# Kernel optimization log

Hardware: AMD Instinct MI355X
Metric: run time of the kernel (lower is better)

Reference implementation:

```python
import jax, jax.numpy as jnp
import numpy as np

B, L, D = 4, 8192, 512


def setup_inputs() -> dict:
    key = jax.random.key(0)
    kx, kwg, kwc = jax.random.split(key, 3)
    x = jax.random.normal(kx, (B, L, D), dtype=jnp.float32)
    # Xavier-uniform init for DxD linears
    bound = float(np.sqrt(6.0 / (D + D)))
    Wg = jax.random.uniform(kwg, (D, D), minval=-bound, maxval=bound, dtype=jnp.float32)
    bg = jnp.ones((D,), dtype=jnp.float32)   # gate bias init to 1.0
    Wc = jax.random.uniform(kwc, (D, D), minval=-bound, maxval=bound, dtype=jnp.float32)
    bc = jnp.zeros((D,), dtype=jnp.float32)
    return {"x": x, "Wg": Wg, "bg": bg, "Wc": Wc, "bc": bc}


def _mingru_scan(gates, cands):
    # h_t = (1 - g_t) * h_{t-1} + g_t * c_t, h_0 = 0
    # linear recurrence h_t = a_t h_{t-1} + b_t with a = 1-g, b = g*c
    a = 1.0 - gates
    b = gates * cands

    def combine(left, right):
        a_l, b_l = left
        a_r, b_r = right
        return a_r * a_l, a_r * b_l + b_r

    _, h = jax.lax.associative_scan(combine, (a, b), axis=1)
    return h


def reference(x, Wg, bg, Wc, bc):
    gates = jax.nn.sigmoid(jnp.einsum('bld,ed->ble', x, Wg) + bg)
    cands = jnp.tanh(jnp.einsum('bld,ed->ble', x, Wc) + bc)
    return _mingru_scan(gates, cands)
```

## Files before the change

kernel.cpp:

```cpp
#include <hip/hip_runtime.h>
#include <stdint.h>
#include <stddef.h>

#define B_ 4
#define L_ 8192
#define D_ 512
#define M_ (B_*L_)
#define K_ 512
#define CHUNK 64
#define NC (L_/CHUNK)

typedef _Float16 f16;
typedef f16 f16x2 __attribute__((ext_vector_type(2)));
typedef f16 f16x4 __attribute__((ext_vector_type(4)));
typedef f16 f16x8 __attribute__((ext_vector_type(8)));
typedef float f32x4 __attribute__((ext_vector_type(4)));

__device__ __forceinline__ void async16(const void* g, void* l) {
  __builtin_amdgcn_global_load_lds(
      (const __attribute__((address_space(1))) uint32_t*)g,
      (__attribute__((address_space(3))) uint32_t*)l,
      16, 0, 0);
}

__global__ __launch_bounds__(256) void prep(const float* __restrict__ x,
                                            const float* __restrict__ Wg,
                                            const float* __restrict__ Wc,
                                            f16* __restrict__ xh,
                                            f16* __restrict__ wp) {
  const int bid = blockIdx.x;
  if (bid < 16384) {
    const int idx = (bid * 256 + threadIdx.x) * 4;
    float4 v = *(const float4*)(x + idx);
    f16x4 o = {(f16)v.x, (f16)v.y, (f16)v.z, (f16)v.w};
    *(f16x4*)(xh + idx) = o;
  } else {
    const int idx = ((bid - 16384) * 256 + threadIdx.x) * 4;
    const float* src = (idx < 262144) ? (Wg + idx) : (Wc + (idx - 262144));
    float4 v = *(const float4*)src;
    f16x4 o = {(f16)v.x, (f16)v.y, (f16)v.z, (f16)v.w};
    *(f16x4*)(wp + idx) = o;
  }
}

__global__ __launch_bounds__(256, 2) void gemm_act(
    const f16* __restrict__ Xh, const f16* __restrict__ Wp,
    const float* __restrict__ bg, const float* __restrict__ bc,
    uint32_t* __restrict__ AC,
    float* __restrict__ cA, float* __restrict__ cB) {
  __shared__ __align__(16) f16 sA[128 * 32];
  __shared__ __align__(16) f16 sBg[128 * 32];
  __shared__ __align__(16) f16 sBc[128 * 32];

  const int tid = threadIdx.x;
  const int id = blockIdx.x;
  const int xcd = id & 7;
  const int slot = id >> 3;
  const int g_ = xcd * 128 + slot;
  const int bm = g_ >> 2;
  const int bn = g_ & 3;

  const int lane = tid & 63;
  const int w = tid >> 6;
  const int wm = w >> 1, wn = w & 1;
  const int l15 = lane & 15, quad = lane >> 4;

  const int srow = tid >> 2;
  const int spc8 = (tid & 3) * 8;
  const f16* gA  = Xh + (size_t)(bm * 128 + srow) * K_ + spc8;
  const f16* gBg = Wp + (size_t)(bn * 128 + srow) * K_ + spc8;
  const f16* gBc = Wp + (size_t)(512 + bn * 128 + srow) * K_ + spc8;
  f16* lA  = sA  + tid * 8;
  f16* lBg = sBg + tid * 8;
  f16* lBc = sBc + tid * 8;

  f32x4 accG[4][4] = {};
  f32x4 accC[4][4] = {};

  for (int k0 = 0; k0 < K_; k0 += 32) {
    async16(gA + k0,  lA);
    async16(gA + (size_t)64 * K_ + k0,  lA  + 64 * 32);
    async16(gBg + k0, lBg);
    async16(gBg + (size_t)64 * K_ + k0, lBg + 64 * 32);
    async16(gBc + k0, lBc);
    async16(gBc + (size_t)64 * K_ + k0, lBc + 64 * 32);
    __syncthreads();

    f16x8 af[4], bgf[4], bcf[4];
#pragma unroll
    for (int i = 0; i < 4; i++)
      af[i]  = *(const f16x8*)(sA  + (wm * 64 + i * 16 + l15) * 32 + quad * 8);
#pragma unroll
    for (int j = 0; j < 4; j++) {
      bgf[j] = *(const f16x8*)(sBg + (wn * 64 + j * 16 + l15) * 32 + quad * 8);
      bcf[j] = *(const f16x8*)(sBc + (wn * 64 + j * 16 + l15) * 32 + quad * 8);
    }
#pragma unroll
    for (int i = 0; i < 4; i++)
#pragma unroll
      for (int j = 0; j < 4; j++) {
        accG[i][j] = __builtin_amdgcn_mfma_f32_16x16x32_f16(af[i], bgf[j], accG[i][j], 0, 0, 0);
        accC[i][j] = __builtin_amdgcn_mfma_f32_16x16x32_f16(af[i], bcf[j], accC[i][j], 0, 0, 0);
      }
    __syncthreads();
  }

  const int c = bm * 2 + wm;
#pragma unroll
  for (int j = 0; j < 4; j++) {
    const int col = bn * 128 + wn * 64 + j * 16 + l15;
    const float bgv = bg[col];
    const float bcv = bc[col];
    float blkP[4], blkQ[4];
#pragma unroll
    for (int i = 0; i < 4; i++) {
      const int mrow = bm * 128 + wm * 64 + i * 16 + quad * 4;
      float P = 1.0f, Q = 0.0f;
#pragma unroll
      for (int r = 0; r < 4; r++) {
        float yg = accG[i][j][r] + bgv;
        float gg = 1.0f / (1.0f + __expf(-yg));
        float yc = accC[i][j][r] + bcv;
        yc = fminf(fmaxf(yc, -15.0f), 15.0f);
        float t = __expf(2.0f * yc);
        float cc = (t - 1.0f) / (t + 1.0f);
        f16x2 p;
        p[0] = (f16)(1.0f - gg);
        p[1] = (f16)(gg * cc);
        *(f16x2*)&AC[(size_t)(mrow + r) * 512 + col] = p;
        const float av = (float)p[0];
        const float bv = (float)p[1];
        Q = fmaf(av, Q, bv);
        P *= av;
      }
      float Pp = __shfl_xor(P, 16);
      float Qp = __shfl_xor(Q, 16);
      float nP = P * Pp;
      float nQ = (quad & 1) ? fmaf(P, Qp, Q) : fmaf(Pp, Q, Qp);
      Pp = __shfl_xor(nP, 32);
      Qp = __shfl_xor(nQ, 32);
      blkP[i] = nP * Pp;
      blkQ[i] = (quad & 2) ? fmaf(nP, Qp, nQ) : fmaf(Pp, nQ, Qp);
    }
    float CP = blkP[0], CQ = blkQ[0];
#pragma unroll
    for (int i = 1; i < 4; i++) {
      CQ = fmaf(blkP[i], CQ, blkQ[i]);
      CP *= blkP[i];
    }
    if (quad == 0) {
      cA[(size_t)c * 512 + col] = CP;
      cB[(size_t)c * 512 + col] = CQ;
    }
  }
}

__global__ __launch_bounds__(256) void scan_apply(
    const uint32_t* __restrict__ AC,
    const float* __restrict__ cA, const float* __restrict__ cB,
    float* __restrict__ out) {
  const int blk = blockIdx.x;
  const int ch = blk & (NC - 1);
  const int bseq = blk >> 7;
  const int d0 = threadIdx.x * 2;

  float h0 = 0.0f, h1 = 0.0f;
  const float* pA = cA + (size_t)(bseq * NC) * 512 + d0;
  const float* pB = cB + (size_t)(bseq * NC) * 512 + d0;
#pragma unroll 4
  for (int cc = 0; cc < ch; cc++) {
    float2 va = *(const float2*)(pA + (size_t)cc * 512);
    float2 vb = *(const float2*)(pB + (size_t)cc * 512);
    h0 = fmaf(va.x, h0, vb.x);
    h1 = fmaf(va.y, h1, vb.y);
  }

  const size_t base = (size_t)blk * CHUNK * 512 + d0;
#pragma unroll 8
  for (int t = 0; t < CHUNK; t++) {
    const size_t i = base + (size_t)t * 512;
    uint2 v = *(const uint2*)&AC[i];
    f16x2 p0 = __builtin_bit_cast(f16x2, v.x);
    f16x2 p1 = __builtin_bit_cast(f16x2, v.y);
    h0 = fmaf((float)p0[0], h0, (float)p0[1]);
    h1 = fmaf((float)p1[0], h1, (float)p1[1]);
    float2 o;
    o.x = h0;
    o.y = h1;
    *(float2*)&out[i] = o;
  }
}

extern "C" void kernel_launch(void* const* d_in, const int* in_sizes, int n_in,
                              void* d_out, int out_size, void* d_ws, size_t ws_size,
                              hipStream_t stream) {
  const float* x  = (const float*)d_in[0];
  const float* Wg = (const float*)d_in[1];
  const float* bg = (const float*)d_in[2];
  const float* Wc = (const float*)d_in[3];
  const float* bc = (const float*)d_in[4];
  float* out = (float*)d_out;

  char* ws = (char*)d_ws;
  f16*      xh = (f16*)(ws);
  f16*      wp = (f16*)(ws + 33554432);
  uint32_t* AC = (uint32_t*)(ws + 34603008);
  float*    cA = (float*)(ws + 101711872);
  float*    cB = (float*)(ws + 102760448);

  prep<<<16896, 256, 0, stream>>>(x, Wg, Wc, xh, wp);
  gemm_act<<<(M_ / 128) * 4, 256, 0, stream>>>(xh, wp, bg, bc, AC, cA, cB);
  scan_apply<<<B_ * NC, 256, 0, stream>>>(AC, cA, cB, out);
}
```

Measured before the change: 208.6 us.

## Fuse x fp32-to-fp16 conversion into GEMM loads and double-buffer LDS tiles

Removes the separate pass that converted x to fp16. The GEMM now loads fp32 x directly into registers, converts it, and writes it to LDS. The K loop is double-buffered: the next tile's loads are issued before the current tile's MFMAs, with manual waitcnt and barriers. This saves a full write and read of the 32MB fp16 x copy, but each GEMM block now reads fp32 x, which is twice the bytes of the fp16 copy, and each tile repeats that read across the 4 column blocks.

```diff
diff --git a/kernel.cpp b/kernel.cpp
--- a/kernel.cpp
+++ b/kernel.cpp
@@ -23,34 +23,24 @@
       16, 0, 0);
 }
 
-__global__ __launch_bounds__(256) void prep(const float* __restrict__ x,
-                                            const float* __restrict__ Wg,
-                                            const float* __restrict__ Wc,
-                                            f16* __restrict__ xh,
-                                            f16* __restrict__ wp) {
-  const int bid = blockIdx.x;
-  if (bid < 16384) {
-    const int idx = (bid * 256 + threadIdx.x) * 4;
-    float4 v = *(const float4*)(x + idx);
-    f16x4 o = {(f16)v.x, (f16)v.y, (f16)v.z, (f16)v.w};
-    *(f16x4*)(xh + idx) = o;
-  } else {
-    const int idx = ((bid - 16384) * 256 + threadIdx.x) * 4;
-    const float* src = (idx < 262144) ? (Wg + idx) : (Wc + (idx - 262144));
-    float4 v = *(const float4*)src;
-    f16x4 o = {(f16)v.x, (f16)v.y, (f16)v.z, (f16)v.w};
-    *(f16x4*)(wp + idx) = o;
-  }
+__global__ __launch_bounds__(256) void prep_w(const float* __restrict__ Wg,
+                                              const float* __restrict__ Wc,
+                                              f16* __restrict__ wp) {
+  const int idx = (blockIdx.x * 256 + threadIdx.x) * 4;
+  const float* src = (idx < 262144) ? (Wg + idx) : (Wc + (idx - 262144));
+  float4 v = *(const float4*)src;
+  f16x4 o = {(f16)v.x, (f16)v.y, (f16)v.z, (f16)v.w};
+  *(f16x4*)(wp + idx) = o;
 }
 
 __global__ __launch_bounds__(256, 2) void gemm_act(
-    const f16* __restrict__ Xh, const f16* __restrict__ Wp,
+    const float* __restrict__ X, const f16* __restrict__ Wp,
     const float* __restrict__ bg, const float* __restrict__ bc,
     uint32_t* __restrict__ AC,
     float* __restrict__ cA, float* __restrict__ cB) {
-  __shared__ __align__(16) f16 sA[128 * 32];
-  __shared__ __align__(16) f16 sBg[128 * 32];
-  __shared__ __align__(16) f16 sBc[128 * 32];
+  __shared__ __align__(16) f16 sA[2][128 * 32];
+  __shared__ __align__(16) f16 sBg[2][128 * 32];
+  __shared__ __align__(16) f16 sBc[2][128 * 32];
 
   const int tid = threadIdx.x;
   const int id = blockIdx.x;
@@ -67,43 +57,66 @@
 
   const int srow = tid >> 2;
   const int spc8 = (tid & 3) * 8;
-  const f16* gA  = Xh + (size_t)(bm * 128 + srow) * K_ + spc8;
+  const float* gx = X + (size_t)(bm * 128 + srow) * K_ + spc8;
   const f16* gBg = Wp + (size_t)(bn * 128 + srow) * K_ + spc8;
   const f16* gBc = Wp + (size_t)(512 + bn * 128 + srow) * K_ + spc8;
-  f16* lA  = sA  + tid * 8;
-  f16* lBg = sBg + tid * 8;
-  f16* lBc = sBc + tid * 8;
 
   f32x4 accG[4][4] = {};
   f32x4 accC[4][4] = {};
 
-  for (int k0 = 0; k0 < K_; k0 += 32) {
-    async16(gA + k0,  lA);
-    async16(gA + (size_t)64 * K_ + k0,  lA  + 64 * 32);
-    async16(gBg + k0, lBg);
-    async16(gBg + (size_t)64 * K_ + k0, lBg + 64 * 32);
-    async16(gBc + k0, lBc);
-    async16(gBc + (size_t)64 * K_ + k0, lBc + 64 * 32);
-    __syncthreads();
-
-    f16x8 af[4], bgf[4], bcf[4];
-#pragma unroll
-    for (int i = 0; i < 4; i++)
-      af[i]  = *(const f16x8*)(sA  + (wm * 64 + i * 16 + l15) * 32 + quad * 8);
-#pragma unroll
-    for (int j = 0; j < 4; j++) {
-      bgf[j] = *(const f16x8*)(sBg + (wn * 64 + j * 16 + l15) * 32 + quad * 8);
-      bcf[j] = *(const f16x8*)(sBc + (wn * 64 + j * 16 + l15) * 32 + quad * 8);
-    }
-#pragma unroll
-    for (int i = 0; i < 4; i++)
-#pragma unroll
-      for (int j = 0; j < 4; j++) {
-        accG[i][j] = __builtin_amdgcn_mfma_f32_16x16x32_f16(af[i], bgf[j], accG[i][j], 0, 0, 0);
-        accC[i][j] = __builtin_amdgcn_mfma_f32_16x16x32_f16(af[i], bcf[j], accC[i][j], 0, 0, 0);
-      }
-    __syncthreads();
-  }
+  float4 ax0, ax1, ax2, ax3;
+
+#define ISSUE(kk, bN) \
+    ax0 = *(const float4*)(gx + (kk)); \
+    ax1 = *(const float4*)(gx + (kk) + 4); \
+    ax2 = *(const float4*)(gx + 64 * K_ + (kk)); \
+    ax3 = *(const float4*)(gx + 64 * K_ + (kk) + 4); \
+    async16(gBg + (kk), &sBg[bN][tid * 8]); \
+    async16(gBg + 64 * K_ + (kk), &sBg[bN][tid * 8 + 64 * 32]); \
+    async16(gBc + (kk), &sBc[bN][tid * 8]); \
+    async16(gBc + 64 * K_ + (kk), &sBc[bN][tid * 8 + 64 * 32]);
+
+#define BODY(kt, bC, bN, DO_ISSUE) { \
+    asm volatile("s_waitcnt vmcnt(0)" ::: "memory"); \
+    f16x8 w0 = {(f16)ax0.x, (f16)ax0.y, (f16)ax0.z, (f16)ax0.w, \
+                (f16)ax1.x, (f16)ax1.y, (f16)ax1.z, (f16)ax1.w}; \
+    f16x8 w1 = {(f16)ax2.x, (f16)ax2.y, (f16)ax2.z, (f16)ax2.w, \
+                (f16)ax3.x, (f16)ax3.y, (f16)ax3.z, (f16)ax3.w}; \
+    *(f16x8*)&sA[bC][tid * 8] = w0; \
+    *(f16x8*)&sA[bC][tid * 8 + 64 * 32] = w1; \
+    if (DO_ISSUE) { ISSUE((kt + 1) * 32, bN); } \
+    asm volatile("s_waitcnt lgkmcnt(0)" ::: "memory"); \
+    __builtin_amdgcn_s_barrier(); \
+    f16x8 af[4], bgf[4], bcf[4]; \
+    _Pragma("unroll") \
+    for (int i = 0; i < 4; i++) \
+      af[i] = *(const f16x8*)(&sA[bC][(wm * 64 + i * 16 + l15) * 32 + quad * 8]); \
+    _Pragma("unroll") \
+    for (int j = 0; j < 4; j++) { \
+      bgf[j] = *(const f16x8*)(&sBg[bC][(wn * 64 + j * 16 + l15) * 32 + quad * 8]); \
+      bcf[j] = *(const f16x8*)(&sBc[bC][(wn * 64 + j * 16 + l15) * 32 + quad * 8]); \
+    } \
+    _Pragma("unroll") \
+    for (int i = 0; i < 4; i++) \
+      _Pragma("unroll") \
+      for (int j = 0; j < 4; j++) { \
+        accG[i][j] = __builtin_amdgcn_mfma_f32_16x16x32_f16(af[i], bgf[j], accG[i][j], 0, 0, 0); \
+        accC[i][j] = __builtin_amdgcn_mfma_f32_16x16x32_f16(af[i], bcf[j], accC[i][j], 0, 0, 0); \
+      } \
+    __builtin_amdgcn_sched_barrier(0); \
+    __builtin_amdgcn_s_barrier(); \
+  }
+
+  ISSUE(0, 0);
+  for (int kt2 = 0; kt2 < 7; kt2++) {
+    const int kt = kt2 * 2;
+    BODY(kt,     0, 1, 1);
+    BODY(kt + 1, 1, 0, 1);
+  }
+  BODY(14, 0, 1, 1);
+  BODY(15, 1, 0, 0);
+#undef BODY
+#undef ISSUE
 
   const int c = bm * 2 + wm;
 #pragma unroll
@@ -202,13 +215,12 @@
   float* out = (float*)d_out;
 
   char* ws = (char*)d_ws;
-  f16*      xh = (f16*)(ws);
-  f16*      wp = (f16*)(ws + 33554432);
-  uint32_t* AC = (uint32_t*)(ws + 34603008);
-  float*    cA = (float*)(ws + 101711872);
-  float*    cB = (float*)(ws + 102760448);
-
-  prep<<<16896, 256, 0, stream>>>(x, Wg, Wc, xh, wp);
-  gemm_act<<<(M_ / 128) * 4, 256, 0, stream>>>(xh, wp, bg, bc, AC, cA, cB);
+  f16*      wp = (f16*)(ws);
+  uint32_t* AC = (uint32_t*)(ws + 1048576);
+  float*    cA = (float*)(ws + 69206016);
+  float*    cB = (float*)(ws + 70254592);
+
+  prep_w<<<512, 256, 0, stream>>>(Wg, Wc, wp);
+  gemm_act<<<(M_ / 128) * 4, 256, 0, stream>>>(x, wp, bg, bc, AC, cA, cB);
   scan_apply<<<B_ * NC, 256, 0, stream>>>(AC, cA, cB, out);
 }
```

Result: no change. 211.3 us (+1.3%).

## Double-buffer LDS tiles in gemm_act to overlap async loads with MFMA

Applied to the files above, without the earlier changes.

Doubles the shared-memory tiles and prefetches the next K-slice via global_load_lds while MFMAs run on the current buffer. One barrier per iteration replaces two, and the K loop is fully unrolled. Shared memory per block doubles to 48KB, which may affect occupancy at two blocks per CU. It also relies on the manual vmcnt wait plus barrier to order LDS reads before the buffer is overwritten.

```diff
diff --git a/kernel.cpp b/kernel.cpp
--- a/kernel.cpp
+++ b/kernel.cpp
@@ -48,9 +48,9 @@
     const float* __restrict__ bg, const float* __restrict__ bc,
     uint32_t* __restrict__ AC,
     float* __restrict__ cA, float* __restrict__ cB) {
-  __shared__ __align__(16) f16 sA[128 * 32];
-  __shared__ __align__(16) f16 sBg[128 * 32];
-  __shared__ __align__(16) f16 sBc[128 * 32];
+  __shared__ __align__(16) f16 sA[2][128 * 32];
+  __shared__ __align__(16) f16 sBg[2][128 * 32];
+  __shared__ __align__(16) f16 sBc[2][128 * 32];
 
   const int tid = threadIdx.x;
   const int id = blockIdx.x;
@@ -70,40 +70,51 @@
   const f16* gA  = Xh + (size_t)(bm * 128 + srow) * K_ + spc8;
   const f16* gBg = Wp + (size_t)(bn * 128 + srow) * K_ + spc8;
   const f16* gBc = Wp + (size_t)(512 + bn * 128 + srow) * K_ + spc8;
-  f16* lA  = sA  + tid * 8;
-  f16* lBg = sBg + tid * 8;
-  f16* lBc = sBc + tid * 8;
 
   f32x4 accG[4][4] = {};
   f32x4 accC[4][4] = {};
 
-  for (int k0 = 0; k0 < K_; k0 += 32) {
-    async16(gA + k0,  lA);
-    async16(gA + (size_t)64 * K_ + k0,  lA  + 64 * 32);
-    async16(gBg + k0, lBg);
-    async16(gBg + (size_t)64 * K_ + k0, lBg + 64 * 32);
-    async16(gBc + k0, lBc);
-    async16(gBc + (size_t)64 * K_ + k0, lBc + 64 * 32);
-    __syncthreads();
-
-    f16x8 af[4], bgf[4], bcf[4];
-#pragma unroll
-    for (int i = 0; i < 4; i++)
-      af[i]  = *(const f16x8*)(sA  + (wm * 64 + i * 16 + l15) * 32 + quad * 8);
-#pragma unroll
-    for (int j = 0; j < 4; j++) {
-      bgf[j] = *(const f16x8*)(sBg + (wn * 64 + j * 16 + l15) * 32 + quad * 8);
-      bcf[j] = *(const f16x8*)(sBc + (wn * 64 + j * 16 + l15) * 32 + quad * 8);
-    }
-#pragma unroll
-    for (int i = 0; i < 4; i++)
-#pragma unroll
-      for (int j = 0; j < 4; j++) {
-        accG[i][j] = __builtin_amdgcn_mfma_f32_16x16x32_f16(af[i], bgf[j], accG[i][j], 0, 0, 0);
-        accC[i][j] = __builtin_amdgcn_mfma_f32_16x16x32_f16(af[i], bcf[j], accC[i][j], 0, 0, 0);
-      }
-    __syncthreads();
-  }
+#define STAGE(kk, b) { \
+    async16(gA + (kk),  &sA[b][tid * 8]); \
+    async16(gA + (size_t)64 * K_ + (kk),  &sA[b][tid * 8 + 64 * 32]); \
+    async16(gBg + (kk), &sBg[b][tid * 8]); \
+    async16(gBg + (size_t)64 * K_ + (kk), &sBg[b][tid * 8 + 64 * 32]); \
+    async16(gBc + (kk), &sBc[b][tid * 8]); \
+    async16(gBc + (size_t)64 * K_ + (kk), &sBc[b][tid * 8 + 64 * 32]); }
+
+#define COMPUTE(bC) { \
+    f16x8 af[4], bgf[4], bcf[4]; \
+    _Pragma("unroll") \
+    for (int i = 0; i < 4; i++) \
+      af[i] = *(const f16x8*)(&sA[bC][(wm * 64 + i * 16 + l15) * 32 + quad * 8]); \
+    _Pragma("unroll") \
+    for (int j = 0; j < 4; j++) { \
+      bgf[j] = *(const f16x8*)(&sBg[bC][(wn * 64 + j * 16 + l15) * 32 + quad * 8]); \
+      bcf[j] = *(const f16x8*)(&sBc[bC][(wn * 64 + j * 16 + l15) * 32 + quad * 8]); \
+    } \
+    _Pragma("unroll") \
+    for (int i = 0; i < 4; i++) \
+      _Pragma("unroll") \
+      for (int j = 0; j < 4; j++) { \
+        accG[i][j] = __builtin_amdgcn_mfma_f32_16x16x32_f16(af[i], bgf[j], accG[i][j], 0, 0, 0); \
+        accC[i][j] = __builtin_amdgcn_mfma_f32_16x16x32_f16(af[i], bcf[j], accC[i][j], 0, 0, 0); \
+      } }
+
+  STAGE(0, 0);
+  asm volatile("s_waitcnt vmcnt(0)" ::: "memory");
+  __builtin_amdgcn_s_barrier();
+
+#pragma unroll
+  for (int t = 0; t < 15; t++) {
+    const int c = t & 1, n = c ^ 1;
+    STAGE((t + 1) * 32, n);
+    COMPUTE(c);
+    asm volatile("s_waitcnt vmcnt(0)" ::: "memory");
+    __builtin_amdgcn_s_barrier();
+  }
+  COMPUTE(1);
+#undef COMPUTE
+#undef STAGE
 
   const int c = bm * 2 + wm;
 #pragma unroll
```

After: 206.8 us. No clear change (-0.9%).
